# Optimization experiments

Hardware: AMD Instinct MI355X
Metric: run time of the kernel (lower is better)

## Reference

```python
import jax, jax.numpy as jnp
import numpy as np


def setup_inputs() -> dict:
    key = jax.random.key(0)
    ks = jax.random.split(key, 6)
    B, C, D, H, O = 4096, 64, 512, 1024, 1
    z = jax.random.normal(ks[0], (B, D), dtype=jnp.float32)
    company_id = jax.random.randint(ks[1], (B,), 0, C)
    # PyTorch Linear default init ~ U(-1/sqrt(fan_in), 1/sqrt(fan_in)); use scaled normals for simplicity
    W1 = jax.random.normal(ks[2], (C, D, H), dtype=jnp.float32) / np.sqrt(D)
    b1 = jax.random.normal(ks[3], (C, H), dtype=jnp.float32) * 0.01
    W2 = jax.random.normal(ks[4], (C, H, O), dtype=jnp.float32) / np.sqrt(H)
    b2 = jax.random.normal(ks[5], (C, O), dtype=jnp.float32) * 0.01
    return {"z": z, "company_id": company_id, "W1": W1, "b1": b1, "W2": W2, "b2": b2}


def reference(z, company_id, W1, b1, W2, b2):
    # Faithful to original: every company head is applied to the full batch,
    # then the single needed row per sample is gathered (dropout is identity in eval).
    # h: [B, C, H]
    h = jnp.einsum("bd,cdh->bch", z, W1) + b1[None, :, :]
    h = jax.nn.gelu(h, approximate=False)  # nn.GELU default = exact erf GELU
    # all_outputs: [B, C, O]
    all_outputs = jnp.einsum("bch,cho->bco", h, W2) + b2[None, :, :]
    # gather the per-sample company row -> [B, O]
    outputs = jnp.take_along_axis(all_outputs, company_id[:, None, None], axis=1)[:, 0, :]
    return outputs
```

## Files before the change

kernel.cpp:

```cpp
#include <hip/hip_runtime.h>

typedef float f32x16 __attribute__((ext_vector_type(16)));
typedef short s16x8  __attribute__((ext_vector_type(8)));

#define B_SZ 4096
#define C_N  64
#define D_K  512
#define H_N  1024
#define BK   16
#define NT   32
#define ROWS 128
#define ZP_OFF_BYTES 32768
#define ZP_ROWS (B_SZ + 128)

__device__ __forceinline__ short f2bf(float f){
  unsigned u = __float_as_uint(f);
  u += 0x7FFFu + ((u >> 16) & 1u);
  return (short)(u >> 16);
}
__device__ __forceinline__ float erf_fast(float x){
  float ax = fabsf(x);
  float t = __builtin_amdgcn_rcpf(1.0f + 0.3275911f * ax);
  float p = t * (0.254829592f + t * (-0.284496736f + t * (1.421413741f +
            t * (-1.453152027f + t * 1.061405429f))));
  float r = 1.0f - p * __expf(-ax * ax);
  return copysignf(r, x);
}
__device__ __forceinline__ float gelu_exact(float x){
  return 0.5f * x * (1.0f + erf_fast(x * 0.70710678118654752f));
}

__global__ void k_cs(const int* __restrict__ cid, int* __restrict__ offsets,
                     int* __restrict__ cursor){
  __shared__ int hist[C_N];
  const int tid = threadIdx.x;
  if (tid < C_N) hist[tid] = 0;
  __syncthreads();
  for (int i = tid; i < B_SZ; i += 1024) atomicAdd(&hist[cid[i]], 1);
  __syncthreads();
  if (tid < 64){
    int v = hist[tid];
    int x = v;
    #pragma unroll
    for (int d = 1; d < 64; d <<= 1){
      int y = __shfl_up(x, d, 64);
      if (tid >= d) x += y;
    }
    offsets[tid] = x - v;
    cursor[tid]  = x - v;
    if (tid == 63) offsets[64] = x;
  }
}

__global__ void k_pack(const int* __restrict__ cid, const float* __restrict__ z,
                       const float* __restrict__ b2, int* __restrict__ cursor,
                       int* __restrict__ bucket, short* __restrict__ zp,
                       float* __restrict__ out){
  __shared__ int pos_s[64];
  const int tid = threadIdx.x;
  const int base = blockIdx.x * 64;
  if (tid < 64){
    int i = base + tid;
    int c = cid[i];
    int p = atomicAdd(&cursor[c], 1);
    pos_s[tid] = p;
    bucket[p] = i;
    out[i] = b2[c];
  }
  __syncthreads();
  #pragma unroll
  for (int j = 0; j < 16; ++j){
    int u = tid + 256 * j;
    int s = u >> 6, oct = u & 63;
    const float* src = z + (size_t)(base + s) * D_K + oct * 8;
    float4 a = *(const float4*)src;
    float4 b = *(const float4*)(src + 4);
    s16x8 v;
    v[0]=f2bf(a.x); v[1]=f2bf(a.y); v[2]=f2bf(a.z); v[3]=f2bf(a.w);
    v[4]=f2bf(b.x); v[5]=f2bf(b.y); v[6]=f2bf(b.z); v[7]=f2bf(b.w);
    *(s16x8*)(zp + ((size_t)pos_s[s] << 9) + oct * 8) = v;
  }
}

__global__ __launch_bounds__(256, 2) void k_main(
    const short* __restrict__ zp, const float* __restrict__ W1,
    const float* __restrict__ b1, const float* __restrict__ W2,
    const int* __restrict__ offsets, const int* __restrict__ bucket,
    float* __restrict__ out)
{
  __shared__ float B_lds[4][BK * 128];
  __shared__ s16x8 A_lds[4][256];
  __shared__ float partial[ROWS];

  const int bid = blockIdx.x;
  const int c = bid & 63, hs = bid >> 6;
  const int off_c = offsets[c];
  const int n_c = offsets[c + 1] - off_c;
  if (n_c == 0) return;

  const int tid  = threadIdx.x;
  const int lane = tid & 63, wave = tid >> 6;
  const int l31 = lane & 31, lhi = lane >> 5;
  const int hcol = hs * 128 + wave * 32 + l31;
  const float b1v = b1[c * H_N + hcol];
  const float w2v = W2[c * H_N + hcol];
  const float* Wpanel = W1 + (size_t)c * D_K * H_N + hs * 128;

  const int r0 = tid >> 5;
  const int hc = (tid & 31) * 4;
  const int arow = ((tid >> 6) << 5) | (tid & 31);
  const int akh  = ((tid >> 5) & 1) * 8;

  if (tid < ROWS) partial[tid] = 0.0f;

  for (int rb = 0; rb < n_c; rb += ROWS){
    const short* zrow = zp + ((size_t)(off_c + rb + arow) << 9) + akh;

    auto stage = [&](int t){
      const int s = t & 3;
      const float* bsrc = Wpanel + (size_t)(t * BK + r0) * H_N + hc;
      __builtin_amdgcn_global_load_lds(
        (const __attribute__((address_space(1))) void*)bsrc,
        (__attribute__((address_space(3))) void*)(&B_lds[s][r0 * 128 + hc]), 16, 0, 0);
      __builtin_amdgcn_global_load_lds(
        (const __attribute__((address_space(1))) void*)(bsrc + 8 * H_N),
        (__attribute__((address_space(3))) void*)(&B_lds[s][(r0 + 8) * 128 + hc]), 16, 0, 0);
      __builtin_amdgcn_global_load_lds(
        (const __attribute__((address_space(1))) void*)(zrow + t * BK),
        (__attribute__((address_space(3))) void*)(&A_lds[s][tid]), 16, 0, 0);
    };

    stage(0); stage(1); stage(2);

    f32x16 acc[4];
    acc[0] = 0; acc[1] = 0; acc[2] = 0; acc[3] = 0;

    for (int t = 0; t < NT; ++t){
      if      (t <  NT - 2) asm volatile("s_waitcnt vmcnt(6)" ::: "memory");
      else if (t == NT - 2) asm volatile("s_waitcnt vmcnt(3)" ::: "memory");
      else                  asm volatile("s_waitcnt vmcnt(0)" ::: "memory");
      __builtin_amdgcn_s_barrier();
      if (t + 3 < NT) stage(t + 3);

      const int s = t & 3;
      const float* Bt = &B_lds[s][0];
      s16x8 bf;
      #pragma unroll
      for (int e = 0; e < 8; ++e)
        bf[e] = f2bf(Bt[(lhi * 8 + e) * 128 + wave * 32 + l31]);
      const s16x8* At = &A_lds[s][0];
      #pragma unroll
      for (int m = 0; m < 4; ++m){
        s16x8 af = At[m * 64 + lane];
        acc[m] = __builtin_amdgcn_mfma_f32_32x32x16_bf16(af, bf, acc[m], 0, 0, 0);
      }
    }

    #pragma unroll
    for (int m = 0; m < 4; ++m){
      #pragma unroll
      for (int r = 0; r < 16; ++r){
        int r_loc = m * 32 + (r & 3) + 8 * (r >> 2) + 4 * lhi;
        float v = gelu_exact(acc[m][r] + b1v) * w2v;
        v += __shfl_xor(v, 1, 64);
        v += __shfl_xor(v, 2, 64);
        v += __shfl_xor(v, 4, 64);
        v += __shfl_xor(v, 8, 64);
        v += __shfl_xor(v, 16, 64);
        if (l31 == 0 && rb + r_loc < n_c)
          atomicAdd(&partial[r_loc], v);
      }
    }
    __syncthreads();
    if (tid < ROWS){
      int g = rb + tid;
      if (g < n_c)
        atomicAdd(&out[bucket[off_c + g]], partial[tid]);
      partial[tid] = 0.0f;
    }
    __syncthreads();
  }
}

extern "C" void kernel_launch(void* const* d_in, const int* in_sizes, int n_in,
                              void* d_out, int out_size, void* d_ws, size_t ws_size,
                              hipStream_t stream){
  const float* z  = (const float*)d_in[0];
  const int*   cid= (const int*)  d_in[1];
  const float* W1 = (const float*)d_in[2];
  const float* b1 = (const float*)d_in[3];
  const float* W2 = (const float*)d_in[4];
  const float* b2 = (const float*)d_in[5];
  float* out = (float*)d_out;

  int*   ws      = (int*)d_ws;
  int*   offsets = ws;
  int*   cursor  = ws + 96;
  int*   bucket  = ws + 192;
  short* zp      = (short*)((char*)d_ws + ZP_OFF_BYTES);

  k_cs   <<<1, 1024, 0, stream>>>(cid, offsets, cursor);
  k_pack <<<64, 256, 0, stream>>>(cid, z, b2, cursor, bucket, zp, out);
  k_main <<<C_N * 8, 256, 0, stream>>>(zp, W1, b1, W2, offsets, bucket, out);
}
```

Before: 58.21 us.

## Halve per-block H slice to double grid size and raise occupancy

Shrinks each block's H column slice from 128 to 64 and launches twice as many blocks. The four waves are regrouped into two row-groups times two column halves, so each wave keeps two MFMA accumulators instead of four. Occupancy is raised to 4 blocks per CU to get more parallelism and memory-latency hiding on the bandwidth-bound W1 stream. The next stage's prefetch is now issued before the barrier, with adjusted vmcnt waits and an extra barrier per iteration to protect LDS slot reuse. In exchange, the packed z rows are re-read by twice as many blocks and each iteration pays one more barrier.

Result: faster. 55.64 us (-4.4%).

```diff
diff --git a/kernel.cpp b/kernel.cpp
--- a/kernel.cpp
+++ b/kernel.cpp
@@ -10,6 +10,7 @@
 #define BK   16
 #define NT   32
 #define ROWS 128
+#define HSLICE 64
 #define ZP_OFF_BYTES 32768
 #define ZP_ROWS (B_SZ + 128)
 
@@ -82,13 +83,13 @@
   }
 }
 
-__global__ __launch_bounds__(256, 2) void k_main(
+__global__ __launch_bounds__(256, 4) void k_main(
     const short* __restrict__ zp, const float* __restrict__ W1,
     const float* __restrict__ b1, const float* __restrict__ W2,
     const int* __restrict__ offsets, const int* __restrict__ bucket,
     float* __restrict__ out)
 {
-  __shared__ float B_lds[4][BK * 128];
+  __shared__ float B_lds[4][BK * HSLICE];
   __shared__ s16x8 A_lds[4][256];
   __shared__ float partial[ROWS];
 
@@ -101,13 +102,14 @@
   const int tid  = threadIdx.x;
   const int lane = tid & 63, wave = tid >> 6;
   const int l31 = lane & 31, lhi = lane >> 5;
-  const int hcol = hs * 128 + wave * 32 + l31;
+  const int wg = wave >> 1, wh = wave & 1;
+  const int hcol = hs * HSLICE + wh * 32 + l31;
   const float b1v = b1[c * H_N + hcol];
   const float w2v = W2[c * H_N + hcol];
-  const float* Wpanel = W1 + (size_t)c * D_K * H_N + hs * 128;
-
-  const int r0 = tid >> 5;
-  const int hc = (tid & 31) * 4;
+  const float* Wpanel = W1 + (size_t)c * D_K * H_N + hs * HSLICE;
+
+  const int brow = tid >> 4;
+  const int bcol = (tid & 15) * 4;
   const int arow = ((tid >> 6) << 5) | (tid & 31);
   const int akh  = ((tid >> 5) & 1) * 8;
 
@@ -118,13 +120,11 @@
 
     auto stage = [&](int t){
       const int s = t & 3;
-      const float* bsrc = Wpanel + (size_t)(t * BK + r0) * H_N + hc;
       __builtin_amdgcn_global_load_lds(
-        (const __attribute__((address_space(1))) void*)bsrc,
-        (__attribute__((address_space(3))) void*)(&B_lds[s][r0 * 128 + hc]), 16, 0, 0);
-      __builtin_amdgcn_global_load_lds(
-        (const __attribute__((address_space(1))) void*)(bsrc + 8 * H_N),
-        (__attribute__((address_space(3))) void*)(&B_lds[s][(r0 + 8) * 128 + hc]), 16, 0, 0);
+        (const __attribute__((address_space(1))) void*)
+          (Wpanel + (size_t)(t * BK + brow) * H_N + bcol),
+        (__attribute__((address_space(3))) void*)(&B_lds[s][brow * HSLICE + bcol]),
+        16, 0, 0);
       __builtin_amdgcn_global_load_lds(
         (const __attribute__((address_space(1))) void*)(zrow + t * BK),
         (__attribute__((address_space(3))) void*)(&A_lds[s][tid]), 16, 0, 0);
@@ -132,36 +132,38 @@
 
     stage(0); stage(1); stage(2);
 
-    f32x16 acc[4];
-    acc[0] = 0; acc[1] = 0; acc[2] = 0; acc[3] = 0;
+    f32x16 acc[2];
+    acc[0] = 0; acc[1] = 0;
 
     for (int t = 0; t < NT; ++t){
-      if      (t <  NT - 2) asm volatile("s_waitcnt vmcnt(6)" ::: "memory");
-      else if (t == NT - 2) asm volatile("s_waitcnt vmcnt(3)" ::: "memory");
+      if (t + 3 < NT) stage(t + 3);
+      if      (t <  NT - 3) asm volatile("s_waitcnt vmcnt(6)" ::: "memory");
+      else if (t == NT - 3) asm volatile("s_waitcnt vmcnt(4)" ::: "memory");
+      else if (t == NT - 2) asm volatile("s_waitcnt vmcnt(2)" ::: "memory");
       else                  asm volatile("s_waitcnt vmcnt(0)" ::: "memory");
       __builtin_amdgcn_s_barrier();
-      if (t + 3 < NT) stage(t + 3);
 
       const int s = t & 3;
       const float* Bt = &B_lds[s][0];
       s16x8 bf;
       #pragma unroll
       for (int e = 0; e < 8; ++e)
-        bf[e] = f2bf(Bt[(lhi * 8 + e) * 128 + wave * 32 + l31]);
+        bf[e] = f2bf(Bt[(lhi * 8 + e) * HSLICE + wh * 32 + l31]);
       const s16x8* At = &A_lds[s][0];
       #pragma unroll
-      for (int m = 0; m < 4; ++m){
-        s16x8 af = At[m * 64 + lane];
-        acc[m] = __builtin_amdgcn_mfma_f32_32x32x16_bf16(af, bf, acc[m], 0, 0, 0);
+      for (int mm = 0; mm < 2; ++mm){
+        s16x8 af = At[(wg * 2 + mm) * 64 + lane];
+        acc[mm] = __builtin_amdgcn_mfma_f32_32x32x16_bf16(af, bf, acc[mm], 0, 0, 0);
       }
+      __builtin_amdgcn_s_barrier();
     }
 
     #pragma unroll
-    for (int m = 0; m < 4; ++m){
+    for (int mm = 0; mm < 2; ++mm){
       #pragma unroll
       for (int r = 0; r < 16; ++r){
-        int r_loc = m * 32 + (r & 3) + 8 * (r >> 2) + 4 * lhi;
-        float v = gelu_exact(acc[m][r] + b1v) * w2v;
+        int r_loc = (wg * 2 + mm) * 32 + (r & 3) + 8 * (r >> 2) + 4 * lhi;
+        float v = gelu_exact(acc[mm][r] + b1v) * w2v;
         v += __shfl_xor(v, 1, 64);
         v += __shfl_xor(v, 2, 64);
         v += __shfl_xor(v, 4, 64);
@@ -201,5 +203,5 @@
 
   k_cs   <<<1, 1024, 0, stream>>>(cid, offsets, cursor);
   k_pack <<<64, 256, 0, stream>>>(cid, z, b2, cursor, bucket, zp, out);
-  k_main <<<C_N * 8, 256, 0, stream>>>(zp, W1, b1, W2, offsets, bucket, out);
-}
+  k_main <<<C_N * 16, 256, 0, stream>>>(zp, W1, b1, W2, offsets, bucket, out);
+}
```

## Widen main-kernel tile to 256 H columns with BK=32 and 3-stage pipeline

Applied to the files above, without the earlier changes.

Each block now has 512 threads covering a 256-wide H slice, halving the grid to 256 blocks. The K step doubles to 32, so each barrier interval issues twice as many MFMAs. The LDS ring shrinks from four stages to three, with loads issued before the wait and a second barrier so a slot is not overwritten while still being read. Each block stages the packed z rows once for twice as many H columns, which halves A reloads. In exchange it adds an extra barrier per step and gives coarser blocks with less scheduling slack.

Measured after the change: 57.26 us. No clear change (-1.6%).

```diff
diff --git a/kernel.cpp b/kernel.cpp
--- a/kernel.cpp
+++ b/kernel.cpp
@@ -7,9 +7,10 @@
 #define C_N  64
 #define D_K  512
 #define H_N  1024
-#define BK   16
-#define NT   32
+#define BK   32
+#define NT   16
 #define ROWS 128
+#define HSLICE 256
 #define ZP_OFF_BYTES 32768
 #define ZP_ROWS (B_SZ + 128)
 
@@ -82,14 +83,14 @@
   }
 }
 
-__global__ __launch_bounds__(256, 2) void k_main(
+__global__ __launch_bounds__(512, 1) void k_main(
     const short* __restrict__ zp, const float* __restrict__ W1,
     const float* __restrict__ b1, const float* __restrict__ W2,
     const int* __restrict__ offsets, const int* __restrict__ bucket,
     float* __restrict__ out)
 {
-  __shared__ float B_lds[4][BK * 128];
-  __shared__ s16x8 A_lds[4][256];
+  __shared__ float B_lds[3][BK * HSLICE];
+  __shared__ s16x8 A_lds[3][512];
   __shared__ float partial[ROWS];
 
   const int bid = blockIdx.x;
@@ -101,59 +102,62 @@
   const int tid  = threadIdx.x;
   const int lane = tid & 63, wave = tid >> 6;
   const int l31 = lane & 31, lhi = lane >> 5;
-  const int hcol = hs * 128 + wave * 32 + l31;
+  const int hcol = hs * HSLICE + wave * 32 + l31;
   const float b1v = b1[c * H_N + hcol];
   const float w2v = W2[c * H_N + hcol];
-  const float* Wpanel = W1 + (size_t)c * D_K * H_N + hs * 128;
-
-  const int r0 = tid >> 5;
-  const int hc = (tid & 31) * 4;
-  const int arow = ((tid >> 6) << 5) | (tid & 31);
-  const int akh  = ((tid >> 5) & 1) * 8;
+  const float* Wpanel = W1 + (size_t)c * D_K * H_N + hs * HSLICE;
+
+  const int arow  = ((tid >> 6) & 3) * 32 + (tid & 31);
+  const int akoff = ((tid >> 8) << 4) | (((tid >> 5) & 1) << 3);
 
   if (tid < ROWS) partial[tid] = 0.0f;
 
   for (int rb = 0; rb < n_c; rb += ROWS){
-    const short* zrow = zp + ((size_t)(off_c + rb + arow) << 9) + akh;
+    const short* zrow = zp + ((size_t)(off_c + rb + arow) << 9) + akoff;
 
     auto stage = [&](int t){
-      const int s = t & 3;
-      const float* bsrc = Wpanel + (size_t)(t * BK + r0) * H_N + hc;
-      __builtin_amdgcn_global_load_lds(
-        (const __attribute__((address_space(1))) void*)bsrc,
-        (__attribute__((address_space(3))) void*)(&B_lds[s][r0 * 128 + hc]), 16, 0, 0);
-      __builtin_amdgcn_global_load_lds(
-        (const __attribute__((address_space(1))) void*)(bsrc + 8 * H_N),
-        (__attribute__((address_space(3))) void*)(&B_lds[s][(r0 + 8) * 128 + hc]), 16, 0, 0);
+      const int sl = t % 3;
+      #pragma unroll
+      for (int s = 0; s < 4; ++s){
+        __builtin_amdgcn_global_load_lds(
+          (const __attribute__((address_space(1))) void*)
+            (Wpanel + (size_t)(t * BK + wave + s * 8) * H_N + (tid & 63) * 4),
+          (__attribute__((address_space(3))) void*)
+            (&B_lds[sl][tid * 4 + s * 2048]), 16, 0, 0);
+      }
       __builtin_amdgcn_global_load_lds(
         (const __attribute__((address_space(1))) void*)(zrow + t * BK),
-        (__attribute__((address_space(3))) void*)(&A_lds[s][tid]), 16, 0, 0);
+        (__attribute__((address_space(3))) void*)(&A_lds[sl][tid]), 16, 0, 0);
     };
 
-    stage(0); stage(1); stage(2);
+    stage(0); stage(1);
 
     f32x16 acc[4];
     acc[0] = 0; acc[1] = 0; acc[2] = 0; acc[3] = 0;
 
     for (int t = 0; t < NT; ++t){
-      if      (t <  NT - 2) asm volatile("s_waitcnt vmcnt(6)" ::: "memory");
-      else if (t == NT - 2) asm volatile("s_waitcnt vmcnt(3)" ::: "memory");
-      else                  asm volatile("s_waitcnt vmcnt(0)" ::: "memory");
+      if (t + 2 < NT) stage(t + 2);
+      if      (t <  NT - 2) asm volatile("s_waitcnt vmcnt(10)" ::: "memory");
+      else if (t == NT - 2) asm volatile("s_waitcnt vmcnt(5)"  ::: "memory");
+      else                  asm volatile("s_waitcnt vmcnt(0)"  ::: "memory");
       __builtin_amdgcn_s_barrier();
-      if (t + 3 < NT) stage(t + 3);
-
-      const int s = t & 3;
-      const float* Bt = &B_lds[s][0];
-      s16x8 bf;
+
+      const int sl = t % 3;
+      const float* Bt = &B_lds[sl][0];
+      const s16x8* At = &A_lds[sl][0];
       #pragma unroll
-      for (int e = 0; e < 8; ++e)
-        bf[e] = f2bf(Bt[(lhi * 8 + e) * 128 + wave * 32 + l31]);
-      const s16x8* At = &A_lds[s][0];
-      #pragma unroll
-      for (int m = 0; m < 4; ++m){
-        s16x8 af = At[m * 64 + lane];
-        acc[m] = __builtin_amdgcn_mfma_f32_32x32x16_bf16(af, bf, acc[m], 0, 0, 0);
+      for (int ks = 0; ks < 2; ++ks){
+        s16x8 bf;
+        #pragma unroll
+        for (int e = 0; e < 8; ++e)
+          bf[e] = f2bf(Bt[(ks * 16 + lhi * 8 + e) * HSLICE + wave * 32 + l31]);
+        #pragma unroll
+        for (int m = 0; m < 4; ++m){
+          s16x8 af = At[ks * 256 + m * 64 + lane];
+          acc[m] = __builtin_amdgcn_mfma_f32_32x32x16_bf16(af, bf, acc[m], 0, 0, 0);
+        }
       }
+      __builtin_amdgcn_s_barrier();
     }
 
     #pragma unroll
@@ -201,5 +205,5 @@
 
   k_cs   <<<1, 1024, 0, stream>>>(cid, offsets, cursor);
   k_pack <<<64, 256, 0, stream>>>(cid, z, b2, cursor, bucket, zp, out);
-  k_main <<<C_N * 8, 256, 0, stream>>>(zp, W1, b1, W2, offsets, bucket, out);
-}
+  k_main <<<C_N * 4, 512, 0, stream>>>(zp, W1, b1, W2, offsets, bucket, out);
+}
```
